# Performance work log

Measured on AMD Instinct MI355X. Metric: run time of the kernel, lower is better.

## Reference

```python
import jax, jax.numpy as jnp
import numpy as np

B, T, HID = 4, 2048, 1024
H, DK, DV, K = 8, 64, 128, 4
EPS = 1e-5


def _dw_causal_conv(x, w, b):
    # x: (B,T,C), w: (C,1,K) depthwise, b: (C,). Causal: left-pad K-1.
    xt = jnp.transpose(x, (0, 2, 1))  # (B,C,T)
    y = jax.lax.conv_general_dilated(
        xt, w, window_strides=(1,), padding=[(K - 1, 0)],
        dimension_numbers=("NCH", "OIH", "NCH"), feature_group_count=x.shape[-1])
    y = y + b[None, :, None]
    return jnp.transpose(y, (0, 2, 1))  # (B,T,C)


def setup_inputs() -> dict:
    key = jax.random.key(0)
    ks = jax.random.split(key, 20)
    s = 0.02
    inp = {
        "x": jax.random.normal(ks[0], (B, T, HID), jnp.float32),
        "Wq": jax.random.normal(ks[1], (H * DK, HID), jnp.float32) * s,
        "Wk": jax.random.normal(ks[2], (H * DK, HID), jnp.float32) * s,
        "Wv": jax.random.normal(ks[3], (H * DV, HID), jnp.float32) * s,
        "Wa": jax.random.normal(ks[4], (H * DV, HID), jnp.float32) * s,
        "ba": jax.random.normal(ks[5], (H * DV,), jnp.float32) * s,
        "Wb": jax.random.normal(ks[6], (H, HID), jnp.float32) * s,
        "bb": jax.random.normal(ks[7], (H,), jnp.float32) * s,
        "Wg": jax.random.normal(ks[8], (H * DV, HID), jnp.float32) * s,
        "Wo": jax.random.normal(ks[9], (HID, H * DV), jnp.float32) * s,
        "qc_w": jax.random.normal(ks[10], (H * DK, 1, K), jnp.float32) * 0.3,
        "qc_b": jnp.zeros((H * DK,), jnp.float32),
        "kc_w": jax.random.normal(ks[11], (H * DK, 1, K), jnp.float32) * 0.3,
        "kc_b": jnp.zeros((H * DK,), jnp.float32),
        "vc_w": jax.random.normal(ks[12], (H * DV, 1, K), jnp.float32) * 0.3,
        "vc_b": jnp.zeros((H * DV,), jnp.float32),
        "ln_w": jnp.ones((DV,), jnp.float32),
        "ln_b": jnp.zeros((DV,), jnp.float32),
    }
    return inp


def _forward(x, Wq, Wk, Wv, Wa, ba, Wb, bb, Wg, Wo,
             qc_w, qc_b, kc_w, kc_b, vc_w, vc_b, ln_w, ln_b):
    b, t = x.shape[0], x.shape[1]
    scale = DK ** -0.5
    q = x @ Wq.T
    k = x @ Wk.T
    v = x @ Wv.T
    q = jax.nn.silu(_dw_causal_conv(q, qc_w, qc_b))
    k = jax.nn.silu(_dw_causal_conv(k, kc_w, kc_b))
    v = jax.nn.silu(_dw_causal_conv(v, vc_w, vc_b))
    q = q.reshape(b, t, H, DK)
    k = (k * scale).reshape(b, t, H, DK)
    v = v.reshape(b, t, H, DV)
    a = jax.nn.sigmoid(x @ Wa.T + ba).reshape(b, t, H, DV)
    beta = jax.nn.sigmoid(x @ Wb.T + bb)  # (B,T,H)

    # gated delta-rule recurrence over time; state S: (B,H,DK,DV)
    def step(S, ins):
        q_t, k_t, v_t, a_t, b_t = ins
        read = jnp.einsum("bhk,bhkv->bhv", k_t, S)          # (B,H,DV)
        err = read - v_t
        S = (a_t[:, :, None, :] * S
             - b_t[:, :, None, None] * k_t[..., None] * err[:, :, None, :])
        o_t = jnp.einsum("bhk,bhkv->bhv", q_t, S)
        return S, o_t

    to_tbh = lambda u: jnp.moveaxis(u, 1, 0)  # (T,B,H,...)
    S0 = jnp.zeros((b, H, DK, DV), x.dtype)
    _, o = jax.lax.scan(step, S0, (to_tbh(q), to_tbh(k), to_tbh(v),
                                   to_tbh(a), to_tbh(beta)))
    o = jnp.moveaxis(o, 0, 1)  # (B,T,H,DV)

    # LayerNorm over DV
    mu = jnp.mean(o, axis=-1, keepdims=True)
    var = jnp.mean((o - mu) ** 2, axis=-1, keepdims=True)
    o = (o - mu) * jax.lax.rsqrt(var + EPS) * ln_w + ln_b

    g = jax.nn.sigmoid(x @ Wg.T).reshape(b, t, H, DV)
    o = (o * g).reshape(b, t, H * DV)
    return o @ Wo.T


def reference(x, Wq, Wk, Wv, Wa, ba, Wb, bb, Wg, Wo,
              qc_w, qc_b, kc_w, kc_b, vc_w, vc_b, ln_w, ln_b):
    return _forward(x, Wq, Wk, Wv, Wa, ba, Wb, bb, Wg, Wo,
                    qc_w, qc_b, kc_w, kc_b, vc_w, vc_b, ln_w, ln_b)
```

## Files before the change

### kernel.cpp

```cpp
#include <hip/hip_runtime.h>
#include <hip/hip_bf16.h>
#include <cstdint>
#include <cstddef>

#define TDIM 2048
#define NH 8

using f32x4 = __attribute__((ext_vector_type(4))) float;
using s16x8 = __attribute__((ext_vector_type(8))) short;

__device__ __forceinline__ float sigm(float x) { return 1.0f / (1.0f + __expf(-x)); }

#define GLDS(gp, lp)                                                          \
    __builtin_amdgcn_global_load_lds(                                         \
        (const __attribute__((address_space(1))) void*)(gp),                  \
        (__attribute__((address_space(3))) void*)(lp), 16, 0, 0)
#define GLDS4(gp, lp)                                                         \
    __builtin_amdgcn_global_load_lds(                                         \
        (const __attribute__((address_space(1))) void*)(gp),                  \
        (__attribute__((address_space(3))) void*)(lp), 4, 0, 0)

template<int CTRL>
__device__ __forceinline__ float dpp_add(float x) {
    int p = __builtin_amdgcn_mov_dpp(__float_as_int(x), CTRL, 0xF, 0xF, true);
    return x + __int_as_float(p);
}
__device__ __forceinline__ float reduce16(float x) {
    x = dpp_add<0xB1>(x);
    x = dpp_add<0x4E>(x);
    x = dpp_add<0x141>(x);
    x = dpp_add<0x140>(x);
    return x;
}

__global__ __launch_bounds__(256) void pack_f32_bf16_kernel(
    const float* __restrict__ src, __hip_bfloat16* __restrict__ dst, int n4)
{
    int i = blockIdx.x * 256 + threadIdx.x;
    if (i >= n4) return;
    float4 v = *(const float4*)(src + (size_t)i * 4);
    size_t o = (size_t)i * 4;
    dst[o + 0] = __float2bfloat16(v.x);
    dst[o + 1] = __float2bfloat16(v.y);
    dst[o + 2] = __float2bfloat16(v.z);
    dst[o + 3] = __float2bfloat16(v.w);
}

__global__ __launch_bounds__(256) void pack_w_kernel(
    const float* __restrict__ Wq, const float* __restrict__ Wk,
    const float* __restrict__ Wv, const float* __restrict__ Wa,
    const float* __restrict__ Wb, const float* __restrict__ Wg,
    __hip_bfloat16* __restrict__ dst)
{
    int e = blockIdx.x * 256 + threadIdx.x;
    int r = e >> 10, c = e & 1023;
    float vv;
    if      (r <  512) vv = Wq[(size_t)r * 1024 + c];
    else if (r < 1024) vv = Wk[(size_t)(r -  512) * 1024 + c];
    else if (r < 2048) vv = Wv[(size_t)(r - 1024) * 1024 + c];
    else if (r < 3072) vv = Wa[(size_t)(r - 2048) * 1024 + c];
    else if (r < 3080) vv = Wb[(size_t)(r - 3072) * 1024 + c];
    else if (r < 4104) vv = Wg[(size_t)(r - 3080) * 1024 + c];
    else               vv = 0.0f;
    dst[e] = __float2bfloat16(vv);
}

__global__ __launch_bounds__(256) void gemm1_kernel(
    const __hip_bfloat16* __restrict__ A, const __hip_bfloat16* __restrict__ Bw,
    float* __restrict__ qraw, float* __restrict__ kraw, float* __restrict__ vraw,
    float* __restrict__ abuf, float* __restrict__ betab, float* __restrict__ gbuf,
    const float* __restrict__ ba, const float* __restrict__ bb)
{
    constexpr int Kd = 1024;
    __shared__ __attribute__((aligned(16))) __hip_bfloat16 At[128 * 32];
    __shared__ __attribute__((aligned(16))) __hip_bfloat16 Bt[128 * 32];
    __shared__ __attribute__((aligned(16))) float Ct[4][16 * 68];
    const int tid = threadIdx.x;
    const int mBase = blockIdx.x * 128;
    const int nBase = blockIdx.y * 128;
    const int wave = tid >> 6, lane = tid & 63;
    const int wm = (wave >> 1) * 64, wn = (wave & 1) * 64;
    const int quad = lane >> 4, l16 = lane & 15;

    f32x4 acc[4][4];
    for (int i = 0; i < 4; i++)
        for (int j = 0; j < 4; j++)
            for (int r = 0; r < 4; r++) acc[i][j][r] = 0.0f;

    const int srow = tid >> 2;
    const int skk = (tid & 3) * 8;
    const __hip_bfloat16* Ag = A + (size_t)(mBase + srow) * Kd + skk;
    const __hip_bfloat16* Bg = Bw + (size_t)(nBase + srow) * Kd + skk;
    __hip_bfloat16* Al = &At[srow * 32 + skk];
    __hip_bfloat16* Bl = &Bt[srow * 32 + skk];

    for (int k0 = 0; k0 < Kd; k0 += 32) {
        GLDS(Ag + k0, Al);
        GLDS(Ag + k0 + (size_t)64 * Kd, Al + 64 * 32);
        GLDS(Bg + k0, Bl);
        GLDS(Bg + k0 + (size_t)64 * Kd, Bl + 64 * 32);
        __syncthreads();
        s16x8 af[4], bfr[4];
#pragma unroll
        for (int i = 0; i < 4; i++)
            af[i] = *(const s16x8*)&At[(wm + i * 16 + l16) * 32 + quad * 8];
#pragma unroll
        for (int j = 0; j < 4; j++)
            bfr[j] = *(const s16x8*)&Bt[(wn + j * 16 + l16) * 32 + quad * 8];
#pragma unroll
        for (int i = 0; i < 4; i++)
#pragma unroll
            for (int j = 0; j < 4; j++)
                acc[i][j] = __builtin_amdgcn_mfma_f32_16x16x32_bf16(af[i], bfr[j], acc[i][j], 0, 0, 0);
        __syncthreads();
    }

    const int ncol = nBase + wn + l16 * 4;
    float* basep; size_t rstr; bool dosig = false; bool skip = false;
    float4 bias = make_float4(0.f, 0.f, 0.f, 0.f);
    if (ncol < 512)       { basep = qraw + ncol;          rstr = 512;  }
    else if (ncol < 1024) { basep = kraw + (ncol - 512);  rstr = 512;  }
    else if (ncol < 2048) { basep = vraw + (ncol - 1024); rstr = 1024; }
    else if (ncol < 3072) { basep = abuf + (ncol - 2048); rstr = 1024; dosig = true;
                            bias = *(const float4*)(ba + (ncol - 2048)); }
    else if (ncol < 3080) { basep = betab + (ncol - 3072); rstr = 8;   dosig = true;
                            bias = *(const float4*)(bb + (ncol - 3072)); }
    else if (ncol < 4104) { basep = gbuf + (ncol - 3080); rstr = 1024; dosig = true; }
    else                  { basep = gbuf; rstr = 0; skip = true; }

#pragma unroll
    for (int i = 0; i < 4; i++) {
#pragma unroll
        for (int j = 0; j < 4; j++)
#pragma unroll
            for (int r = 0; r < 4; r++)
                Ct[wave][(quad * 4 + r) * 68 + j * 16 + l16] = acc[i][j][r];
        __syncthreads();
#pragma unroll
        for (int p = 0; p < 4; p++) {
            int rr = p * 4 + quad;
            float4 val = *(const float4*)&Ct[wave][rr * 68 + l16 * 4];
            if (dosig) {
                val.x = sigm(val.x + bias.x);
                val.y = sigm(val.y + bias.y);
                val.z = sigm(val.z + bias.z);
                val.w = sigm(val.w + bias.w);
            }
            int m = mBase + wm + i * 16 + rr;
            if (!skip) *(float4*)(basep + (size_t)m * rstr) = val;
        }
        __syncthreads();
    }
}

__global__ __launch_bounds__(256) void gemm2_kernel(
    const __hip_bfloat16* __restrict__ A, const __hip_bfloat16* __restrict__ Bw,
    float* __restrict__ out)
{
    constexpr int Kd = 1024;
    __shared__ __attribute__((aligned(16))) __hip_bfloat16 At[128 * 32];
    __shared__ __attribute__((aligned(16))) __hip_bfloat16 Bt[128 * 32];
    __shared__ __attribute__((aligned(16))) float Ct[4][16 * 68];
    const int tid = threadIdx.x;
    const int mBase = blockIdx.x * 128;
    const int nBase = blockIdx.y * 128;
    const int wave = tid >> 6, lane = tid & 63;
    const int wm = (wave >> 1) * 64, wn = (wave & 1) * 64;
    const int quad = lane >> 4, l16 = lane & 15;

    f32x4 acc[4][4];
    for (int i = 0; i < 4; i++)
        for (int j = 0; j < 4; j++)
            for (int r = 0; r < 4; r++) acc[i][j][r] = 0.0f;

    const int srow = tid >> 2;
    const int skk = (tid & 3) * 8;
    const __hip_bfloat16* Ag = A + (size_t)(mBase + srow) * Kd + skk;
    const __hip_bfloat16* Bg = Bw + (size_t)(nBase + srow) * Kd + skk;
    __hip_bfloat16* Al = &At[srow * 32 + skk];
    __hip_bfloat16* Bl = &Bt[srow * 32 + skk];

    for (int k0 = 0; k0 < Kd; k0 += 32) {
        GLDS(Ag + k0, Al);
        GLDS(Ag + k0 + (size_t)64 * Kd, Al + 64 * 32);
        GLDS(Bg + k0, Bl);
        GLDS(Bg + k0 + (size_t)64 * Kd, Bl + 64 * 32);
        __syncthreads();
        s16x8 af[4], bfr[4];
#pragma unroll
        for (int i = 0; i < 4; i++)
            af[i] = *(const s16x8*)&At[(wm + i * 16 + l16) * 32 + quad * 8];
#pragma unroll
        for (int j = 0; j < 4; j++)
            bfr[j] = *(const s16x8*)&Bt[(wn + j * 16 + l16) * 32 + quad * 8];
#pragma unroll
        for (int i = 0; i < 4; i++)
#pragma unroll
            for (int j = 0; j < 4; j++)
                acc[i][j] = __builtin_amdgcn_mfma_f32_16x16x32_bf16(af[i], bfr[j], acc[i][j], 0, 0, 0);
        __syncthreads();
    }

    const int ncol = nBase + wn + l16 * 4;
    float* basep = out + ncol;
#pragma unroll
    for (int i = 0; i < 4; i++) {
#pragma unroll
        for (int j = 0; j < 4; j++)
#pragma unroll
            for (int r = 0; r < 4; r++)
                Ct[wave][(quad * 4 + r) * 68 + j * 16 + l16] = acc[i][j][r];
        __syncthreads();
#pragma unroll
        for (int p = 0; p < 4; p++) {
            int rr = p * 4 + quad;
            float4 val = *(const float4*)&Ct[wave][rr * 68 + l16 * 4];
            int m = mBase + wm + i * 16 + rr;
            *(float4*)(basep + (size_t)m * 1024) = val;
        }
        __syncthreads();
    }
}

__global__ __launch_bounds__(256) void conv_silu_fused_kernel(
    const float* __restrict__ qraw, const float* __restrict__ kraw,
    const float* __restrict__ vraw,
    const float* __restrict__ qw, const float* __restrict__ qb,
    const float* __restrict__ kw, const float* __restrict__ kb,
    const float* __restrict__ vw, const float* __restrict__ vb,
    float* __restrict__ qcb, float* __restrict__ kcb, float* __restrict__ vcb)
{
    int e = blockIdx.x * 256 + threadIdx.x;
    int c = e & 2047;
    int bt4 = e >> 11;
    int t0 = (bt4 & 511) * 4;
    int bb_ = bt4 >> 9;
    const float* src; float* dst; const float* w4; const float* bi;
    int C, cc; float scale = 1.0f;
    if (c < 512)       { src = qraw; dst = qcb; w4 = qw; bi = qb; C = 512;  cc = c; }
    else if (c < 1024) { src = kraw; dst = kcb; w4 = kw; bi = kb; C = 512;  cc = c - 512; scale = 0.125f; }
    else               { src = vraw; dst = vcb; w4 = vw; bi = vb; C = 1024; cc = c - 1024; }
    const float* wc = w4 + (size_t)cc * 4;
    const float w0 = wc[0], w1 = wc[1], w2 = wc[2], w3 = wc[3];
    const float bs = bi[cc];
    const float* s = src + ((size_t)bb_ * TDIM + t0) * C + cc;
    float x0, x1, x2;
    if (t0 == 0) { x0 = 0.f; x1 = 0.f; x2 = 0.f; }
    else { x0 = s[-3 * C]; x1 = s[-2 * C]; x2 = s[-C]; }
    const float x3 = s[0], x4 = s[C], x5 = s[2 * C], x6 = s[3 * C];
    float* d = dst + ((size_t)bb_ * TDIM + t0) * C + cc;
    float y;
    y = fmaf(w0, x0, fmaf(w1, x1, fmaf(w2, x2, fmaf(w3, x3, bs))));
    d[0] = y * sigm(y) * scale;
    y = fmaf(w0, x1, fmaf(w1, x2, fmaf(w2, x3, fmaf(w3, x4, bs))));
    d[C] = y * sigm(y) * scale;
    y = fmaf(w0, x2, fmaf(w1, x3, fmaf(w2, x4, fmaf(w3, x5, bs))));
    d[2 * C] = y * sigm(y) * scale;
    y = fmaf(w0, x3, fmaf(w1, x4, fmaf(w2, x5, fmaf(w3, x6, bs))));
    d[3 * C] = y * sigm(y) * scale;
}

#define CH 32
#define NCHUNK (TDIM / CH)

#define SCAN_STAGE_KQ(BUF, T0) do {                                           \
    _Pragma("unroll") for (int j = 0; j < 8; j++) {                           \
        int flat = j * 64 + lane;                                             \
        int tt = flat >> 4, c4 = (flat & 15) * 4;                             \
        GLDS(kc + kqB + (size_t)((T0) + tt) * 512 + c4, &kL[BUF][j * 256]);   \
        GLDS(qc + kqB + (size_t)((T0) + tt) * 512 + c4, &qL[BUF][j * 256]);   \
    }                                                                         \
} while (0)

#define LOADOPS(BUF, TT, SL) do {                                             \
    kR[SL] = *(const float4*)&kL[BUF][(TT) * 64 + ks * 4];                    \
    qR[SL] = *(const float4*)&qL[BUF][(TT) * 64 + ks * 4];                    \
    vabR[SL] = *(const float4*)&vabL[BUF][((TT) * 4 + vi) * 4];               \
} while (0)

#define CSTEP(SL, TT) do {                                                    \
    const float4 kk = kR[SL];                                                 \
    const float4 qq = qR[SL];                                                 \
    const float VV = vabR[SL].x, AA = vabR[SL].y, BB = vabR[SL].z;            \
    float as0 = AA * S0, as1 = AA * S1, as2 = AA * S2, as3 = AA * S3;         \
    float nbv = VV * (-BB);                                                   \
    float r0 = kk.x * S0, r1 = kk.y * S1;                                     \
    r0 = fmaf(kk.z, S2, r0); r1 = fmaf(kk.w, S3, r1);                         \
    float rr = reduce16(r0 + r1);                                             \
    float cc = fmaf(BB, rr, nbv);                                             \
    S0 = fmaf(-cc, kk.x, as0); float o0 = qq.x * S0;                          \
    S1 = fmaf(-cc, kk.y, as1); float o1 = qq.y * S1;                          \
    S2 = fmaf(-cc, kk.z, as2); o0 = fmaf(qq.z, S2, o0);                       \
    S3 = fmaf(-cc, kk.w, as3); o1 = fmaf(qq.w, S3, o1);                       \
    oacc[TT] = reduce16(o0 + o1);                                             \
} while (0)

__global__ __launch_bounds__(64) void scan_kernel(
    const float* __restrict__ qc, const float* __restrict__ kc,
    const float* __restrict__ vc, const float* __restrict__ ab,
    const float* __restrict__ betab, float* __restrict__ ob)
{
    __shared__ __attribute__((aligned(16))) float kL[2][CH * 64];
    __shared__ __attribute__((aligned(16))) float qL[2][CH * 64];
    __shared__ __attribute__((aligned(16))) float vabL[2][CH * 4 * 4];
    __shared__ __attribute__((aligned(16))) float oL[4 * CH];

    const int bid = blockIdx.x;
    const int bh = bid & 31, vg = bid >> 5;
    const int h = bh & 7, b = bh >> 3;
    const int lane = threadIdx.x;
    const int ks = lane & 15, vi = lane >> 4;

    const size_t kqB = (size_t)b * TDIM * 512 + (size_t)h * 64;
    const size_t vaB = (size_t)b * TDIM * 1024 + (size_t)h * 128 + (size_t)vg * 4;
    const size_t beB = (size_t)b * TDIM * 8 + h;

    const int t0p = lane >> 2, c0p = lane & 3;
    const int t1p = 16 + t0p;

    float S0 = 0, S1 = 0, S2 = 0, S3 = 0;
    float4 kR[4], qR[4], vabR[4];
    float oacc[CH];

    SCAN_STAGE_KQ(0, 0);
    {
        float v0 = vc[vaB + (size_t)t0p * 1024 + c0p];
        float a0 = ab[vaB + (size_t)t0p * 1024 + c0p];
        float e0 = betab[beB + (size_t)t0p * 8];
        float v1 = vc[vaB + (size_t)t1p * 1024 + c0p];
        float a1 = ab[vaB + (size_t)t1p * 1024 + c0p];
        float e1 = betab[beB + (size_t)t1p * 8];
        *(float4*)&vabL[0][lane * 4] = make_float4(v0, a0, e0, 0.f);
        *(float4*)&vabL[0][(64 + lane) * 4] = make_float4(v1, a1, e1, 0.f);
    }
    __syncthreads();
    LOADOPS(0, 0, 0); LOADOPS(0, 1, 1); LOADOPS(0, 2, 2); LOADOPS(0, 3, 3);

    for (int chk = 0; chk < NCHUNK; chk++) {
        const int buf = chk & 1;
        const int nb = buf ^ 1;
        const int tn = (chk + 1 < NCHUNK) ? (chk + 1) * CH : 0;
        SCAN_STAGE_KQ(nb, tn);
        const float nv0 = vc[vaB + (size_t)(tn + t0p) * 1024 + c0p];
        const float na0 = ab[vaB + (size_t)(tn + t0p) * 1024 + c0p];
        const float ne0 = betab[beB + (size_t)(tn + t0p) * 8];
        const float nv1 = vc[vaB + (size_t)(tn + t1p) * 1024 + c0p];
        const float na1 = ab[vaB + (size_t)(tn + t1p) * 1024 + c0p];
        const float ne1 = betab[beB + (size_t)(tn + t1p) * 8];
#pragma unroll
        for (int t = 0; t < CH; t++) {
            CSTEP(t & 3, t);
            if (t + 4 < CH) LOADOPS(buf, t + 4, t & 3);
        }
        *(float4*)&vabL[nb][lane * 4] = make_float4(nv0, na0, ne0, 0.f);
        *(float4*)&vabL[nb][(64 + lane) * 4] = make_float4(nv1, na1, ne1, 0.f);
        if (ks == 0) {
#pragma unroll
            for (int j = 0; j < 8; j++) {
                float4 o4 = make_float4(oacc[j * 4], oacc[j * 4 + 1],
                                        oacc[j * 4 + 2], oacc[j * 4 + 3]);
                *(float4*)&oL[vi * CH + j * 4] = o4;
            }
        }
        __syncthreads();
        if (lane < CH) {
            float4 ov = make_float4(oL[0 * CH + lane], oL[1 * CH + lane],
                                    oL[2 * CH + lane], oL[3 * CH + lane]);
            *(float4*)(ob + vaB + (size_t)(chk * CH + lane) * 1024) = ov;
        }
        LOADOPS(nb, 0, 0); LOADOPS(nb, 1, 1); LOADOPS(nb, 2, 2); LOADOPS(nb, 3, 3);
    }
}

__global__ __launch_bounds__(256) void ln_gate_kernel(
    const float* __restrict__ ob, const float* __restrict__ g,
    const float* __restrict__ lnw, const float* __restrict__ lnb,
    __hip_bfloat16* __restrict__ opr)
{
    int row = blockIdx.x * 4 + (threadIdx.x >> 6);
    int lane = threadIdx.x & 63;
    size_t base = (size_t)row * 128 + lane * 2;
    float2 xv = *(const float2*)(ob + base);
    float s = xv.x + xv.y;
#pragma unroll
    for (int m = 1; m <= 32; m <<= 1) s += __shfl_xor(s, m);
    float mean = s * (1.0f / 128.0f);
    float d0 = xv.x - mean, d1 = xv.y - mean;
    float vs = d0 * d0 + d1 * d1;
#pragma unroll
    for (int m = 1; m <= 32; m <<= 1) vs += __shfl_xor(vs, m);
    float rstd = rsqrtf(vs * (1.0f / 128.0f) + 1e-5f);
    float2 gv = *(const float2*)(g + base);
    float w0 = lnw[lane * 2], w1 = lnw[lane * 2 + 1];
    float b0 = lnb[lane * 2], b1 = lnb[lane * 2 + 1];
    opr[base] = __float2bfloat16((d0 * rstd * w0 + b0) * gv.x);
    opr[base + 1] = __float2bfloat16((d1 * rstd * w1 + b1) * gv.y);
}

extern "C" void kernel_launch(void* const* d_in, const int* in_sizes, int n_in,
                              void* d_out, int out_size, void* d_ws, size_t ws_size,
                              hipStream_t stream)
{
    const float* x    = (const float*)d_in[0];
    const float* Wq   = (const float*)d_in[1];
    const float* Wk   = (const float*)d_in[2];
    const float* Wv   = (const float*)d_in[3];
    const float* Wa   = (const float*)d_in[4];
    const float* ba   = (const float*)d_in[5];
    const float* Wb   = (const float*)d_in[6];
    const float* bb   = (const float*)d_in[7];
    const float* Wg   = (const float*)d_in[8];
    const float* Wo   = (const float*)d_in[9];
    const float* qc_w = (const float*)d_in[10];
    const float* qc_b = (const float*)d_in[11];
    const float* kc_w = (const float*)d_in[12];
    const float* kc_b = (const float*)d_in[13];
    const float* vc_w = (const float*)d_in[14];
    const float* vc_b = (const float*)d_in[15];
    const float* ln_w = (const float*)d_in[16];
    const float* ln_b = (const float*)d_in[17];
    float* out = (float*)d_out;

    char* W = (char*)d_ws;
    __hip_bfloat16* xbf  = (__hip_bfloat16*)(W + 0);
    __hip_bfloat16* wcat = (__hip_bfloat16*)(W + 16777216);
    __hip_bfloat16* wobf = (__hip_bfloat16*)(W + 25427968);
    float* qraw  = (float*)(W + 27525120);
    float* kraw  = (float*)(W + 44302336);
    float* vraw  = (float*)(W + 61079552);
    float* abuf  = (float*)(W + 94633984);
    float* betab = (float*)(W + 128188416);
    float* gbuf  = (float*)(W + 128450560);
    float* kcb   = (float*)(W + 162004992);
    float* vcb   = (float*)(W + 178782208);
    float* qcb   = (float*)xbf;
    float* obuf  = (float*)qraw;
    __hip_bfloat16* opr = (__hip_bfloat16*)vraw;

    pack_f32_bf16_kernel<<<8192, 256, 0, stream>>>(x, xbf, 2097152);
    pack_w_kernel<<<16896, 256, 0, stream>>>(Wq, Wk, Wv, Wa, Wb, Wg, wcat);
    pack_f32_bf16_kernel<<<1024, 256, 0, stream>>>(Wo, wobf, 262144);
    gemm1_kernel<<<dim3(64, 33), 256, 0, stream>>>(xbf, wcat, qraw, kraw, vraw,
                                                   abuf, betab, gbuf, ba, bb);
    conv_silu_fused_kernel<<<16384, 256, 0, stream>>>(
        qraw, kraw, vraw, qc_w, qc_b, kc_w, kc_b, vc_w, vc_b, qcb, kcb, vcb);
    scan_kernel<<<1024, 64, 0, stream>>>(qcb, kcb, vcb, abuf, betab, obuf);
    ln_gate_kernel<<<16384, 256, 0, stream>>>(obuf, gbuf, ln_w, ln_b, opr);
    gemm2_kernel<<<dim3(64, 8), 256, 0, stream>>>(opr, wobf, out);
}
```

Measured before the change: 536.2 us.

## Pair scan steps algebraically to shorten the serial reduction chain

Two recurrence steps are now processed together. The second step's read k2·S is rewritten from the pre-update state using the k2·k1 dot product, so the three cross-lane reductions for a pair run in parallel instead of serially. The output reductions are moved out of the step loop and batched after each chunk. This shortens the per-step dependency chain through DPP reductions in a latency-bound scan. The cost is extra FMAs and reductions per pair, and small floating-point reassociation differences.

```diff
diff --git a/kernel.cpp b/kernel.cpp
--- a/kernel.cpp
+++ b/kernel.cpp
@@ -278,21 +278,32 @@
     vabR[SL] = *(const float4*)&vabL[BUF][((TT) * 4 + vi) * 4];               \
 } while (0)
 
-#define CSTEP(SL, TT) do {                                                    \
-    const float4 kk = kR[SL];                                                 \
-    const float4 qq = qR[SL];                                                 \
-    const float VV = vabR[SL].x, AA = vabR[SL].y, BB = vabR[SL].z;            \
-    float as0 = AA * S0, as1 = AA * S1, as2 = AA * S2, as3 = AA * S3;         \
-    float nbv = VV * (-BB);                                                   \
-    float r0 = kk.x * S0, r1 = kk.y * S1;                                     \
-    r0 = fmaf(kk.z, S2, r0); r1 = fmaf(kk.w, S3, r1);                         \
-    float rr = reduce16(r0 + r1);                                             \
-    float cc = fmaf(BB, rr, nbv);                                             \
-    S0 = fmaf(-cc, kk.x, as0); float o0 = qq.x * S0;                          \
-    S1 = fmaf(-cc, kk.y, as1); float o1 = qq.y * S1;                          \
-    S2 = fmaf(-cc, kk.z, as2); o0 = fmaf(qq.z, S2, o0);                       \
-    S3 = fmaf(-cc, kk.w, as3); o1 = fmaf(qq.w, S3, o1);                       \
-    oacc[TT] = reduce16(o0 + o1);                                             \
+#define CPAIR(SLA, SLB, TA) do {                                              \
+    const float4 k1 = kR[SLA], q1 = qR[SLA];                                  \
+    const float4 k2 = kR[SLB], q2 = qR[SLB];                                  \
+    const float V1 = vabR[SLA].x, A1 = vabR[SLA].y, B1 = vabR[SLA].z;         \
+    const float V2 = vabR[SLB].x, A2 = vabR[SLB].y, B2 = vabR[SLB].z;         \
+    float u1 = k1.x * S0, u2 = k2.x * S0, g21 = k2.x * k1.x;                  \
+    u1 = fmaf(k1.y, S1, u1); u2 = fmaf(k2.y, S1, u2);                         \
+    g21 = fmaf(k2.y, k1.y, g21);                                              \
+    u1 = fmaf(k1.z, S2, u1); u2 = fmaf(k2.z, S2, u2);                         \
+    g21 = fmaf(k2.z, k1.z, g21);                                              \
+    u1 = fmaf(k1.w, S3, u1); u2 = fmaf(k2.w, S3, u2);                         \
+    g21 = fmaf(k2.w, k1.w, g21);                                              \
+    u1 = reduce16(u1); u2 = reduce16(u2); g21 = reduce16(g21);                \
+    const float c1 = B1 * (u1 - V1);                                          \
+    S0 = fmaf(-c1, k1.x, A1 * S0); float o0 = q1.x * S0;                      \
+    S1 = fmaf(-c1, k1.y, A1 * S1); float o1 = q1.y * S1;                      \
+    S2 = fmaf(-c1, k1.z, A1 * S2); o0 = fmaf(q1.z, S2, o0);                   \
+    S3 = fmaf(-c1, k1.w, A1 * S3); o1 = fmaf(q1.w, S3, o1);                   \
+    oacc[TA] = o0 + o1;                                                       \
+    const float u2p = fmaf(A1, u2, -(c1 * g21));                              \
+    const float c2 = B2 * (u2p - V2);                                         \
+    S0 = fmaf(-c2, k2.x, A2 * S0); float p0 = q2.x * S0;                      \
+    S1 = fmaf(-c2, k2.y, A2 * S1); float p1 = q2.y * S1;                      \
+    S2 = fmaf(-c2, k2.z, A2 * S2); p0 = fmaf(q2.z, S2, p0);                   \
+    S3 = fmaf(-c2, k2.w, A2 * S3); p1 = fmaf(q2.w, S3, p1);                   \
+    oacc[(TA) + 1] = p0 + p1;                                                 \
 } while (0)
 
 __global__ __launch_bounds__(64) void scan_kernel(
@@ -348,10 +359,15 @@
         const float na1 = ab[vaB + (size_t)(tn + t1p) * 1024 + c0p];
         const float ne1 = betab[beB + (size_t)(tn + t1p) * 8];
 #pragma unroll
-        for (int t = 0; t < CH; t++) {
-            CSTEP(t & 3, t);
-            if (t + 4 < CH) LOADOPS(buf, t + 4, t & 3);
+        for (int t = 0; t < CH; t += 2) {
+            CPAIR(t & 3, (t + 1) & 3, t);
+            if (t + 4 < CH) {
+                LOADOPS(buf, t + 4, t & 3);
+                LOADOPS(buf, t + 5, (t + 1) & 3);
+            }
         }
+#pragma unroll
+        for (int j = 0; j < CH; j++) oacc[j] = reduce16(oacc[j]);
         *(float4*)&vabL[nb][lane * 4] = make_float4(nv0, na0, ne0, 0.f);
         *(float4*)&vabL[nb][(64 + lane) * 4] = make_float4(nv1, na1, ne1, 0.f);
         if (ks == 0) {
```

After: 549.2 us. 1.02x slower.
